# Kernel tuning notes

Hardware: AMD Instinct MI355X
Metric: run time of the kernel (lower is better)

## Reference

```python
import jax, jax.numpy as jnp
import numpy as np

NUM_HEADS = 16
HEAD_DIM = 128  # d_out / num_heads = 2048 / 16
WINDOW = 2048   # sliding_window_size


def setup_inputs() -> dict:
    key = jax.random.key(0)
    kx, kq, kk, kv, ko = jax.random.split(key, 5)
    b, s, d = 2, 2048, 2048
    scale = 0.02
    return {
        "x": jax.random.normal(kx, (b, s, d), dtype=jnp.float32),
        "Wq": jax.random.normal(kq, (d, d), dtype=jnp.float32) * scale,
        "Wk": jax.random.normal(kk, (d, d), dtype=jnp.float32) * scale,
        "Wv": jax.random.normal(kv, (d, d), dtype=jnp.float32) * scale,
        "Wo": jax.random.normal(ko, (d, d), dtype=jnp.float32) * scale,
    }


def reference(x, Wq, Wk, Wv, Wo):
    b, s, _ = x.shape
    H, Dh, W = NUM_HEADS, HEAD_DIM, WINDOW

    # qkv projections (no bias), split into heads: [b, s, H, Dh]
    q = (x @ Wq).reshape(b, s, H, Dh)
    k = (x @ Wk).reshape(b, s, H, Dh)
    v = (x @ Wv).reshape(b, s, H, Dh)

    # attn scores: [b, H, q, k]
    scores = jnp.einsum("bqhd,bkhd->bhqk", q, k)

    # sliding-window mask from absolute positions (fresh cache: q_start=k_start=0)
    pos = jnp.arange(s)
    diff = pos[:, None] - pos[None, :]  # q_pos - k_pos
    mask = (diff < 0) | (diff >= W)
    scores = jnp.where(mask[None, None], -jnp.inf, scores)

    attn = jax.nn.softmax(scores / np.sqrt(Dh).astype(np.float32), axis=-1)

    # context: [b, s, H, Dh] -> [b, s, d_out]
    ctx = jnp.einsum("bhqk,bkhd->bqhd", attn, v).reshape(b, s, H * Dh)
    return ctx @ Wo
```

## Files before the change

kernel.cpp:

```cpp
#include <hip/hip_runtime.h>

typedef __bf16 bf16;
typedef __bf16 bf16x4 __attribute__((ext_vector_type(4)));
typedef __bf16 bf16x8 __attribute__((ext_vector_type(8)));
typedef float f32x4 __attribute__((ext_vector_type(4)));

#define B_ 2
#define S_ 2048
#define D_ 2048
#define H_ 16
#define DH_ 128
#define QKVN 6144

__device__ __forceinline__ void async_load16(const bf16* g, bf16* l) {
    __builtin_amdgcn_global_load_lds((const __attribute__((address_space(1))) void*)g,
                                     (__attribute__((address_space(3))) void*)l, 16, 0, 0);
}

__device__ __forceinline__ unsigned int bf16_bits(float x) {
    bf16 h = (bf16)x;
    return (unsigned int)__builtin_bit_cast(unsigned short, h);
}

__global__ __launch_bounds__(256) void cvt_kernel(const float* __restrict__ src,
                                                  bf16* __restrict__ dst) {
    size_t i = (size_t)blockIdx.x * 256 + threadIdx.x;
    const float4* s = (const float4*)src;
    float4 a = s[2 * i], b = s[2 * i + 1];
    bf16x8 o;
    o[0] = (bf16)a.x; o[1] = (bf16)a.y; o[2] = (bf16)a.z; o[3] = (bf16)a.w;
    o[4] = (bf16)b.x; o[5] = (bf16)b.y; o[6] = (bf16)b.z; o[7] = (bf16)b.w;
    *(bf16x8*)(dst + 8 * i) = o;
}

__global__ __launch_bounds__(256) void wtrans_kernel(const float* __restrict__ Wq,
                                                     const float* __restrict__ Wk,
                                                     const float* __restrict__ Wv,
                                                     const float* __restrict__ Wo,
                                                     bf16* __restrict__ WqkvT,
                                                     bf16* __restrict__ WoT) {
    __shared__ unsigned int tile[64][65];
    int z = blockIdx.z;
    const float* src = (z == 0) ? Wq : (z == 1) ? Wk : (z == 2) ? Wv : Wo;
    bf16* dst = (z < 3) ? (WqkvT + (size_t)z * D_ * D_) : WoT;
    int r0 = blockIdx.y * 64, c0 = blockIdx.x * 64;
    int t = threadIdx.x;
    int tr = t >> 4, tc4 = (t & 15) * 4;
#pragma unroll
    for (int it = 0; it < 4; ++it) {
        int r = it * 16 + tr;
        float4 v = *(const float4*)(src + (size_t)(r0 + r) * D_ + c0 + tc4);
        tile[r][tc4 + 0] = bf16_bits(v.x);
        tile[r][tc4 + 1] = bf16_bits(v.y);
        tile[r][tc4 + 2] = bf16_bits(v.z);
        tile[r][tc4 + 3] = bf16_bits(v.w);
    }
    __syncthreads();
#pragma unroll
    for (int it = 0; it < 4; ++it) {
        int a = it * 16 + tr;
        unsigned u0 = tile[tc4 + 0][a], u1 = tile[tc4 + 1][a];
        unsigned u2 = tile[tc4 + 2][a], u3 = tile[tc4 + 3][a];
        uint2 v;
        v.x = (u0 & 0xffffu) | (u1 << 16);
        v.y = (u2 & 0xffffu) | (u3 << 16);
        *(uint2*)(dst + (size_t)(c0 + a) * D_ + r0 + tc4) = v;
    }
}

__global__ __launch_bounds__(256) void vtrans_kernel(const bf16* __restrict__ qkv,
                                                     bf16* __restrict__ vt) {
    __shared__ unsigned int tile[64][65];
    int bh = blockIdx.z;
    int b = bh >> 4, h = bh & 15;
    int s0 = blockIdx.x * 64, d0 = blockIdx.y * 64;
    int t = threadIdx.x, tr = t >> 4, tc4 = (t & 15) * 4;
#pragma unroll
    for (int it = 0; it < 4; ++it) {
        int r = it * 16 + tr;
        uint2 v = *(const uint2*)(qkv + (size_t)(b * S_ + s0 + r) * QKVN + 2 * D_ + h * DH_ + d0 + tc4);
        tile[r][tc4 + 0] = v.x & 0xffffu;
        tile[r][tc4 + 1] = v.x >> 16;
        tile[r][tc4 + 2] = v.y & 0xffffu;
        tile[r][tc4 + 3] = v.y >> 16;
    }
    __syncthreads();
#pragma unroll
    for (int it = 0; it < 4; ++it) {
        int a = it * 16 + tr;
        unsigned u0 = tile[tc4 + 0][a], u1 = tile[tc4 + 1][a];
        unsigned u2 = tile[tc4 + 2][a], u3 = tile[tc4 + 3][a];
        uint2 v;
        v.x = (u0 & 0xffffu) | (u1 << 16);
        v.y = (u2 & 0xffffu) | (u3 << 16);
        *(uint2*)(vt + (size_t)bh * DH_ * S_ + (size_t)(d0 + a) * S_ + s0 + tc4) = v;
    }
}

template <typename CT>
__global__ __launch_bounds__(256) void gemm_bt(const bf16* __restrict__ A,
                                               const bf16* __restrict__ Bt,
                                               CT* __restrict__ C,
                                               int M, int N, int K) {
    __shared__ __align__(16) bf16 As[128 * 32];
    __shared__ __align__(16) bf16 Bs[128 * 32];
    int t = threadIdx.x;
    int w = t >> 6, l = t & 63;
    int quad = l >> 4, lr = l & 15;
    int wr = w >> 1, wc = w & 1;
    size_t m0 = (size_t)blockIdx.y * 128, n0 = (size_t)blockIdx.x * 128;
    int srow = l >> 2, scol = (l & 3) * 8;

    f32x4 acc[4][4];
#pragma unroll
    for (int i = 0; i < 4; ++i)
#pragma unroll
        for (int j = 0; j < 4; ++j) acc[i][j] = (f32x4){0.f, 0.f, 0.f, 0.f};

    for (int k0 = 0; k0 < K; k0 += 32) {
        __syncthreads();
#pragma unroll
        for (int i = 0; i < 2; ++i) {
            int c = w * 2 + i;
            async_load16(A + (m0 + c * 16 + srow) * (size_t)K + k0 + scol, As + c * 512);
            async_load16(Bt + (n0 + c * 16 + srow) * (size_t)K + k0 + scol, Bs + c * 512);
        }
        asm volatile("s_waitcnt vmcnt(0)" ::: "memory");
        __syncthreads();
        bf16x8 af[4], bfr[4];
#pragma unroll
        for (int i = 0; i < 4; ++i) af[i] = *(const bf16x8*)(As + (wr * 64 + i * 16 + lr) * 32 + quad * 8);
#pragma unroll
        for (int j = 0; j < 4; ++j) bfr[j] = *(const bf16x8*)(Bs + (wc * 64 + j * 16 + lr) * 32 + quad * 8);
#pragma unroll
        for (int i = 0; i < 4; ++i)
#pragma unroll
            for (int j = 0; j < 4; ++j)
                acc[i][j] = __builtin_amdgcn_mfma_f32_16x16x32_bf16(af[i], bfr[j], acc[i][j], 0, 0, 0);
    }

    size_t bm = m0 + wr * 64 + quad * 4;
    size_t bn = n0 + wc * 64 + lr;
#pragma unroll
    for (int i = 0; i < 4; ++i)
#pragma unroll
        for (int j = 0; j < 4; ++j)
#pragma unroll
            for (int r = 0; r < 4; ++r)
                C[(bm + i * 16 + r) * (size_t)N + bn + j * 16] = (CT)acc[i][j][r];
}

#define QK_K 2048
#define QK_N 6144

__device__ __forceinline__ bf16x8 lds_frag(const bf16* tile, int row, int colByte) {
    int off = row * 128 + (colByte ^ ((row & 7) << 4));
    return *(const bf16x8*)((const char*)tile + off);
}

template <int MH, int NH>
__device__ __forceinline__ void mmaq8(f32x4 (&acc)[8][4], const bf16x8 (&afr)[4][2],
                                      const bf16x8 (&bf)[2][2]) {
    __builtin_amdgcn_s_setprio(1);
#pragma unroll
    for (int i = 0; i < 4; ++i)
#pragma unroll
        for (int j = 0; j < 2; ++j)
#pragma unroll
            for (int kk = 0; kk < 2; ++kk)
                acc[MH * 4 + i][NH * 2 + j] = __builtin_amdgcn_mfma_f32_16x16x32_bf16(
                    afr[i][kk], bf[j][kk], acc[MH * 4 + i][NH * 2 + j], 0, 0, 0);
    __builtin_amdgcn_s_setprio(0);
}

__global__ __launch_bounds__(512, 2) void gemm_qkv(const bf16* __restrict__ A,
                                                   const bf16* __restrict__ Bt,
                                                   bf16* __restrict__ C) {
    __shared__ __align__(16) bf16 As[2][256 * 64];
    __shared__ __align__(16) bf16 Bs[2][256 * 64];

    int t = threadIdx.x;
    int wid = t >> 6, lane = t & 63;
    int quad = lane >> 4, lr = lane & 15;
    int wr = wid >> 2, wn = wid & 3;

    int bid = blockIdx.x;
    int swz = (bid & 7) * 48 + (bid >> 3);
    int tn = swz >> 4, tm = swz & 15;
    size_t m0 = (size_t)tm * 256, n0 = (size_t)tn * 256;

    int row_r[2], c8s_r[2];
#pragma unroll
    for (int r = 0; r < 2; ++r) {
        int idx = r * 512 + t;
        row_r[r] = idx >> 3;
        c8s_r[r] = (idx & 7) ^ (row_r[r] & 7);
    }

    auto stA = [&](int kt, int bufi, int h) {
#pragma unroll
        for (int r = 0; r < 2; ++r)
            async_load16(A + (m0 + h * 128 + row_r[r]) * (size_t)QK_K + kt * 64 + c8s_r[r] * 8,
                         &As[bufi][(h * 1024 + r * 512 + wid * 64) * 8]);
    };
    auto stB = [&](int kt, int bufi, int h) {
#pragma unroll
        for (int r = 0; r < 2; ++r)
            async_load16(Bt + (n0 + h * 128 + row_r[r]) * (size_t)QK_K + kt * 64 + c8s_r[r] * 8,
                         &Bs[bufi][(h * 1024 + r * 512 + wid * 64) * 8]);
    };

    f32x4 acc[8][4];
#pragma unroll
    for (int i = 0; i < 8; ++i)
#pragma unroll
        for (int j = 0; j < 4; ++j) acc[i][j] = (f32x4){0.f, 0.f, 0.f, 0.f};

    bf16x8 afr[4][2], bf0[2][2], bf1[2][2];

    auto readA = [&](int bufi, int mh) {
#pragma unroll
        for (int i = 0; i < 4; ++i)
#pragma unroll
            for (int kk = 0; kk < 2; ++kk)
                afr[i][kk] = lds_frag(As[bufi], mh * 128 + wr * 64 + i * 16 + lr, kk * 64 + quad * 16);
    };
    auto readB = [&](int bufi, int nh, bf16x8 (&bf)[2][2]) {
#pragma unroll
        for (int j = 0; j < 2; ++j)
#pragma unroll
            for (int kk = 0; kk < 2; ++kk)
                bf[j][kk] = lds_frag(Bs[bufi], nh * 128 + wn * 32 + j * 16 + lr, kk * 64 + quad * 16);
    };

    stA(0, 0, 0); stB(0, 0, 0); stB(0, 0, 1); stA(0, 0, 1);
    asm volatile("s_waitcnt vmcnt(4)" ::: "memory");
    stA(1, 1, 0); stB(1, 1, 0); stB(1, 1, 1);
    asm volatile("s_waitcnt vmcnt(6)" ::: "memory");
    __builtin_amdgcn_s_barrier();

    for (int it2 = 0; it2 < 15; ++it2) {
        int tt = 2 * it2;
        readA(0, 0);
        readB(0, 0, bf0);
        stA(tt + 1, 1, 1);
        __builtin_amdgcn_s_barrier();
        asm volatile("s_waitcnt lgkmcnt(0)" ::: "memory");
        __builtin_amdgcn_sched_barrier(0);
        mmaq8<0, 0>(acc, afr, bf0);
        __builtin_amdgcn_s_barrier();
        readB(0, 1, bf1);
        stA(tt + 2, 0, 0);
        __builtin_amdgcn_s_barrier();
        asm volatile("s_waitcnt lgkmcnt(0)" ::: "memory");
        __builtin_amdgcn_sched_barrier(0);
        mmaq8<0, 1>(acc, afr, bf1);
        __builtin_amdgcn_s_barrier();
        readA(0, 1);
        stB(tt + 2, 0, 0);
        __builtin_amdgcn_s_barrier();
        asm volatile("s_waitcnt lgkmcnt(0)" ::: "memory");
        __builtin_amdgcn_sched_barrier(0);
        mmaq8<1, 0>(acc, afr, bf0);
        __builtin_amdgcn_s_barrier();
        stB(tt + 2, 0, 1);
        asm volatile("s_waitcnt vmcnt(6)" ::: "memory");
        __builtin_amdgcn_s_barrier();
        mmaq8<1, 1>(acc, afr, bf1);
        __builtin_amdgcn_s_barrier();
        readA(1, 0);
        readB(1, 0, bf0);
        stA(tt + 2, 0, 1);
        __builtin_amdgcn_s_barrier();
        asm volatile("s_waitcnt lgkmcnt(0)" ::: "memory");
        __builtin_amdgcn_sched_barrier(0);
        mmaq8<0, 0>(acc, afr, bf0);
        __builtin_amdgcn_s_barrier();
        readB(1, 1, bf1);
        stA(tt + 3, 1, 0);
        __builtin_amdgcn_s_barrier();
        asm volatile("s_waitcnt lgkmcnt(0)" ::: "memory");
        __builtin_amdgcn_sched_barrier(0);
        mmaq8<0, 1>(acc, afr, bf1);
        __builtin_amdgcn_s_barrier();
        readA(1, 1);
        stB(tt + 3, 1, 0);
        __builtin_amdgcn_s_barrier();
        asm volatile("s_waitcnt lgkmcnt(0)" ::: "memory");
        __builtin_amdgcn_sched_barrier(0);
        mmaq8<1, 0>(acc, afr, bf0);
        __builtin_amdgcn_s_barrier();
        stB(tt + 3, 1, 1);
        asm volatile("s_waitcnt vmcnt(6)" ::: "memory");
        __builtin_amdgcn_s_barrier();
        mmaq8<1, 1>(acc, afr, bf1);
        __builtin_amdgcn_s_barrier();
    }

    {
        readA(0, 0);
        readB(0, 0, bf0);
        stA(31, 1, 1);
        __builtin_amdgcn_s_barrier();
        asm volatile("s_waitcnt lgkmcnt(0)" ::: "memory");
        __builtin_amdgcn_sched_barrier(0);
        mmaq8<0, 0>(acc, afr, bf0);
        __builtin_amdgcn_s_barrier();
        readB(0, 1, bf1);
        __builtin_amdgcn_s_barrier();
        asm volatile("s_waitcnt lgkmcnt(0)" ::: "memory");
        __builtin_amdgcn_sched_barrier(0);
        mmaq8<0, 1>(acc, afr, bf1);
        __builtin_amdgcn_s_barrier();
        readA(0, 1);
        __builtin_amdgcn_s_barrier();
        asm volatile("s_waitcnt lgkmcnt(0)" ::: "memory");
        __builtin_amdgcn_sched_barrier(0);
        mmaq8<1, 0>(acc, afr, bf0);
        __builtin_amdgcn_s_barrier();
        asm volatile("s_waitcnt vmcnt(0)" ::: "memory");
        __builtin_amdgcn_s_barrier();
        mmaq8<1, 1>(acc, afr, bf1);
        __builtin_amdgcn_s_barrier();
        readA(1, 0);
        readB(1, 0, bf0);
        asm volatile("s_waitcnt lgkmcnt(0)" ::: "memory");
        __builtin_amdgcn_sched_barrier(0);
        mmaq8<0, 0>(acc, afr, bf0);
        readB(1, 1, bf1);
        asm volatile("s_waitcnt lgkmcnt(0)" ::: "memory");
        __builtin_amdgcn_sched_barrier(0);
        mmaq8<0, 1>(acc, afr, bf1);
        readA(1, 1);
        asm volatile("s_waitcnt lgkmcnt(0)" ::: "memory");
        __builtin_amdgcn_sched_barrier(0);
        mmaq8<1, 0>(acc, afr, bf0);
        mmaq8<1, 1>(acc, afr, bf1);
    }

#pragma unroll
    for (int mh = 0; mh < 2; ++mh)
#pragma unroll
        for (int i = 0; i < 4; ++i)
#pragma unroll
            for (int nh = 0; nh < 2; ++nh)
#pragma unroll
                for (int j = 0; j < 2; ++j)
#pragma unroll
                    for (int r = 0; r < 4; ++r) {
                        size_t row = m0 + mh * 128 + wr * 64 + i * 16 + quad * 4 + r;
                        size_t col = n0 + nh * 128 + wn * 32 + j * 16 + lr;
                        C[row * QK_N + col] = (bf16)acc[mh * 4 + i][nh * 2 + j][r];
                    }
}

__global__ __launch_bounds__(128) void attn_kernel(const bf16* __restrict__ qkv,
                                                   const bf16* __restrict__ vt,
                                                   bf16* __restrict__ ctx) {
    __shared__ __align__(16) bf16 Ks[2][64 * 128];
    __shared__ __align__(16) bf16 Vts[2][128 * 64];
    __shared__ __align__(16) bf16 Ps[2][32][68];

    int y = blockIdx.y;
    int p = blockIdx.x;
    int b = y >> 4, h = y & 15;
    int t = threadIdx.x, w = t >> 6, l = t & 63;
    int quad = l >> 4, lr = l & 15;

    const bf16* qbase = qkv + (size_t)b * S_ * QKVN + h * DH_;
    const bf16* kbase = qbase + D_;
    const bf16* vbase = vt + (size_t)y * DH_ * S_;

    const int qtA = p, qtB = 31 - p;
    const int nA = p + 1;

    auto stage = [&](int kt, int bi) {
#pragma unroll
        for (int ii = 0; ii < 8; ++ii) {
            int i = 8 * w + ii;
            int row = 4 * i + (l >> 4);
            int cl = (l & 15) ^ (row & 7);
            async_load16(kbase + (size_t)(kt * 64 + row) * QKVN + cl * 8, Ks[bi] + i * 512);
        }
#pragma unroll
        for (int ii = 0; ii < 8; ++ii) {
            int i = 8 * w + ii;
            int dh = 8 * i + (l >> 3);
            int cl = (l & 7) ^ (dh & 7);
            async_load16(vbase + (size_t)dh * S_ + kt * 64 + cl * 8, Vts[bi] + i * 512);
        }
    };

    const float sc2 = 0.12751745f;

    int qt = qtA, q0 = qt * 64;
    bf16x8 qf[2][4];
    auto loadQ = [&]() {
#pragma unroll
        for (int g = 0; g < 2; ++g)
#pragma unroll
            for (int kk = 0; kk < 4; ++kk) {
                bf16x8 raw = *(const bf16x8*)(qbase + (size_t)(q0 + w * 32 + g * 16 + lr) * QKVN + kk * 32 + quad * 8);
#pragma unroll
                for (int e = 0; e < 8; ++e) qf[g][kk][e] = (bf16)((float)raw[e] * sc2);
            }
    };
    loadQ();

    float L_r[2][4];
    f32x4 o[2][8];
#pragma unroll
    for (int g = 0; g < 2; ++g) {
#pragma unroll
        for (int r = 0; r < 4; ++r) L_r[g][r] = 0.f;
#pragma unroll
        for (int nt = 0; nt < 8; ++nt) o[g][nt] = (f32x4){0.f, 0.f, 0.f, 0.f};
    }

    auto epilogue = [&](int q0e) {
#pragma unroll
        for (int g = 0; g < 2; ++g) {
#pragma unroll
            for (int d = 1; d < 16; d <<= 1)
#pragma unroll
                for (int r = 0; r < 4; ++r) L_r[g][r] += __shfl_xor(L_r[g][r], d, 64);
#pragma unroll
            for (int r = 0; r < 4; ++r) {
                float inv = __builtin_amdgcn_rcpf(L_r[g][r]);
                int q = q0e + w * 32 + g * 16 + quad * 4 + r;
#pragma unroll
                for (int nt = 0; nt < 8; ++nt)
                    ctx[(size_t)(b * S_ + q) * D_ + h * DH_ + nt * 16 + lr] = (bf16)(o[g][nt][r] * inv);
            }
        }
    };

    stage(0, 0);

    for (int it = 0; it < 33; ++it) {
        int buf = it & 1;
        asm volatile("s_waitcnt vmcnt(0)" ::: "memory");
        __syncthreads();
        if (it + 1 < 33) {
            int nit = it + 1;
            int nkt = (nit < nA) ? nit : (nit - nA);
            stage(nkt, buf ^ 1);
        }
        int kt = (it < nA) ? it : (it - nA);

        f32x4 s[2][4];
#pragma unroll
        for (int g = 0; g < 2; ++g)
#pragma unroll
            for (int jt = 0; jt < 4; ++jt) s[g][jt] = (f32x4){0.f, 0.f, 0.f, 0.f};
#pragma unroll
        for (int kk = 0; kk < 4; ++kk)
#pragma unroll
            for (int jt = 0; jt < 4; ++jt) {
                bf16x8 kf = *(const bf16x8*)(Ks[buf] + (jt * 16 + lr) * 128 + ((4 * kk + quad) ^ (lr & 7)) * 8);
                s[0][jt] = __builtin_amdgcn_mfma_f32_16x16x32_bf16(qf[0][kk], kf, s[0][jt], 0, 0, 0);
                s[1][jt] = __builtin_amdgcn_mfma_f32_16x16x32_bf16(qf[1][kk], kf, s[1][jt], 0, 0, 0);
            }

        bool diag = (kt == qt);
#pragma unroll
        for (int g = 0; g < 2; ++g) {
#pragma unroll
            for (int jt = 0; jt < 4; ++jt) {
                int keyi = jt * 16 + lr;
#pragma unroll
                for (int r = 0; r < 4; ++r) {
                    float s2 = s[g][jt][r];
                    if (diag && keyi > w * 32 + g * 16 + quad * 4 + r) s2 = -3.0e38f;
                    float pv = __builtin_amdgcn_exp2f(s2);
                    s[g][jt][r] = pv;
                    L_r[g][r] += pv;
                }
            }
#pragma unroll
            for (int jt = 0; jt < 4; ++jt)
#pragma unroll
                for (int r = 0; r < 4; ++r)
                    Ps[w][g * 16 + quad * 4 + r][jt * 16 + lr] = (bf16)s[g][jt][r];
        }
        asm volatile("s_waitcnt lgkmcnt(0)" ::: "memory");

#pragma unroll
        for (int ks = 0; ks < 2; ++ks) {
            bf16x8 pf[2];
#pragma unroll
            for (int g = 0; g < 2; ++g) {
                const bf16* pp = &Ps[w][g * 16 + lr][ks * 32 + quad * 8];
                bf16x4 lo = *(const bf16x4*)pp;
                bf16x4 hi = *(const bf16x4*)(pp + 4);
                pf[g] = __builtin_shufflevector(lo, hi, 0, 1, 2, 3, 4, 5, 6, 7);
            }
#pragma unroll
            for (int nt = 0; nt < 8; ++nt) {
                bf16x8 vf = *(const bf16x8*)(Vts[buf] + (nt * 16 + lr) * 64 + ((4 * ks + quad) ^ (lr & 7)) * 8);
                o[0][nt] = __builtin_amdgcn_mfma_f32_16x16x32_bf16(pf[0], vf, o[0][nt], 0, 0, 0);
                o[1][nt] = __builtin_amdgcn_mfma_f32_16x16x32_bf16(pf[1], vf, o[1][nt], 0, 0, 0);
            }
        }

        if (it == nA - 1) {
            epilogue(q0);
            qt = qtB;
            q0 = qt * 64;
            loadQ();
#pragma unroll
            for (int g = 0; g < 2; ++g) {
#pragma unroll
                for (int r = 0; r < 4; ++r) L_r[g][r] = 0.f;
#pragma unroll
                for (int nt = 0; nt < 8; ++nt) o[g][nt] = (f32x4){0.f, 0.f, 0.f, 0.f};
            }
        }
    }

    epilogue(q0);
}

extern "C" void kernel_launch(void* const* d_in, const int* in_sizes, int n_in,
                              void* d_out, int out_size, void* d_ws, size_t ws_size,
                              hipStream_t stream) {
    const float* x  = (const float*)d_in[0];
    const float* Wq = (const float*)d_in[1];
    const float* Wk = (const float*)d_in[2];
    const float* Wv = (const float*)d_in[3];
    const float* Wo = (const float*)d_in[4];
    float* out = (float*)d_out;

    char* ws = (char*)d_ws;
    bf16* WqkvT = (bf16*)(ws);
    bf16* WoT   = (bf16*)(ws + 25165824);
    bf16* qkv   = (bf16*)(ws + 33554432);
    bf16* vt    = (bf16*)(ws + 83886080);
    bf16* ctx   = (bf16*)(ws + 100663296);
    bf16* xb    = (bf16*)(ws + 117440512);

    cvt_kernel<<<4096, 256, 0, stream>>>(x, xb);
    wtrans_kernel<<<dim3(32, 32, 4), 256, 0, stream>>>(Wq, Wk, Wv, Wo, WqkvT, WoT);
    gemm_qkv<<<dim3(384), 512, 0, stream>>>(xb, WqkvT, qkv);
    vtrans_kernel<<<dim3(32, 2, 32), 256, 0, stream>>>(qkv, vt);
    attn_kernel<<<dim3(16, 32), 128, 0, stream>>>(qkv, vt, ctx);
    gemm_bt<float><<<dim3(16, 32), 256, 0, stream>>>(ctx, WoT, out, B_ * S_, D_, D_);
}
```

Before: 411.8 us.

## Split attention block work across four waves with 16 query rows each

The attention kernel now launches 256 threads (4 waves) per block instead of 128. Each wave handles 16 query rows instead of 32, and the K/V staging loads are spread across twice as many threads. This halves the per-wave register footprint for the O accumulators and scores, which should raise occupancy and latency hiding. In exchange each K/V fragment read from LDS feeds half as many MFMAs, so LDS read traffic per FLOP goes up. An unused NKT constant was also added in the GEMM.

```diff
diff --git a/kernel.cpp b/kernel.cpp
--- a/kernel.cpp
+++ b/kernel.cpp
@@ -239,6 +239,7 @@
     asm volatile("s_waitcnt vmcnt(6)" ::: "memory");
     __builtin_amdgcn_s_barrier();
 
+    const int NKT = QK_K / 64;
     for (int it2 = 0; it2 < 15; ++it2) {
         int tt = 2 * it2;
         readA(0, 0);
@@ -354,12 +355,12 @@
                     }
 }
 
-__global__ __launch_bounds__(128) void attn_kernel(const bf16* __restrict__ qkv,
-                                                   const bf16* __restrict__ vt,
-                                                   bf16* __restrict__ ctx) {
+__global__ __launch_bounds__(256, 2) void attn_kernel(const bf16* __restrict__ qkv,
+                                                      const bf16* __restrict__ vt,
+                                                      bf16* __restrict__ ctx) {
     __shared__ __align__(16) bf16 Ks[2][64 * 128];
     __shared__ __align__(16) bf16 Vts[2][128 * 64];
-    __shared__ __align__(16) bf16 Ps[2][32][68];
+    __shared__ __align__(16) bf16 Ps[4][16][68];
 
     int y = blockIdx.y;
     int p = blockIdx.x;
@@ -376,15 +377,15 @@
 
     auto stage = [&](int kt, int bi) {
 #pragma unroll
-        for (int ii = 0; ii < 8; ++ii) {
-            int i = 8 * w + ii;
+        for (int ii = 0; ii < 4; ++ii) {
+            int i = 4 * w + ii;
             int row = 4 * i + (l >> 4);
             int cl = (l & 15) ^ (row & 7);
             async_load16(kbase + (size_t)(kt * 64 + row) * QKVN + cl * 8, Ks[bi] + i * 512);
         }
 #pragma unroll
-        for (int ii = 0; ii < 8; ++ii) {
-            int i = 8 * w + ii;
+        for (int ii = 0; ii < 4; ++ii) {
+            int i = 4 * w + ii;
             int dh = 8 * i + (l >> 3);
             int cl = (l & 7) ^ (dh & 7);
             async_load16(vbase + (size_t)dh * S_ + kt * 64 + cl * 8, Vts[bi] + i * 512);
@@ -394,44 +395,36 @@
     const float sc2 = 0.12751745f;
 
     int qt = qtA, q0 = qt * 64;
-    bf16x8 qf[2][4];
+    bf16x8 qf[4];
     auto loadQ = [&]() {
 #pragma unroll
-        for (int g = 0; g < 2; ++g)
-#pragma unroll
-            for (int kk = 0; kk < 4; ++kk) {
-                bf16x8 raw = *(const bf16x8*)(qbase + (size_t)(q0 + w * 32 + g * 16 + lr) * QKVN + kk * 32 + quad * 8);
-#pragma unroll
-                for (int e = 0; e < 8; ++e) qf[g][kk][e] = (bf16)((float)raw[e] * sc2);
-            }
+        for (int kk = 0; kk < 4; ++kk) {
+            bf16x8 raw = *(const bf16x8*)(qbase + (size_t)(q0 + w * 16 + lr) * QKVN + kk * 32 + quad * 8);
+#pragma unroll
+            for (int e = 0; e < 8; ++e) qf[kk][e] = (bf16)((float)raw[e] * sc2);
+        }
     };
     loadQ();
 
-    float L_r[2][4];
-    f32x4 o[2][8];
-#pragma unroll
-    for (int g = 0; g < 2; ++g) {
-#pragma unroll
-        for (int r = 0; r < 4; ++r) L_r[g][r] = 0.f;
-#pragma unroll
-        for (int nt = 0; nt < 8; ++nt) o[g][nt] = (f32x4){0.f, 0.f, 0.f, 0.f};
-    }
+    float L_r[4];
+    f32x4 o[8];
+#pragma unroll
+    for (int r = 0; r < 4; ++r) L_r[r] = 0.f;
+#pragma unroll
+    for (int nt = 0; nt < 8; ++nt) o[nt] = (f32x4){0.f, 0.f, 0.f, 0.f};
 
     auto epilogue = [&](int q0e) {
 #pragma unroll
-        for (int g = 0; g < 2; ++g) {
-#pragma unroll
-            for (int d = 1; d < 16; d <<= 1)
-#pragma unroll
-                for (int r = 0; r < 4; ++r) L_r[g][r] += __shfl_xor(L_r[g][r], d, 64);
-#pragma unroll
-            for (int r = 0; r < 4; ++r) {
-                float inv = __builtin_amdgcn_rcpf(L_r[g][r]);
-                int q = q0e + w * 32 + g * 16 + quad * 4 + r;
-#pragma unroll
-                for (int nt = 0; nt < 8; ++nt)
-                    ctx[(size_t)(b * S_ + q) * D_ + h * DH_ + nt * 16 + lr] = (bf16)(o[g][nt][r] * inv);
-            }
+        for (int d = 1; d < 16; d <<= 1)
+#pragma unroll
+            for (int r = 0; r < 4; ++r) L_r[r] += __shfl_xor(L_r[r], d, 64);
+#pragma unroll
+        for (int r = 0; r < 4; ++r) {
+            float inv = __builtin_amdgcn_rcpf(L_r[r]);
+            int q = q0e + w * 16 + quad * 4 + r;
+#pragma unroll
+            for (int nt = 0; nt < 8; ++nt)
+                ctx[(size_t)(b * S_ + q) * D_ + h * DH_ + nt * 16 + lr] = (bf16)(o[nt][r] * inv);
         }
     };
 
@@ -448,58 +441,47 @@
         }
         int kt = (it < nA) ? it : (it - nA);
 
-        f32x4 s[2][4];
-#pragma unroll
-        for (int g = 0; g < 2; ++g)
-#pragma unroll
-            for (int jt = 0; jt < 4; ++jt) s[g][jt] = (f32x4){0.f, 0.f, 0.f, 0.f};
+        f32x4 s[4];
+#pragma unroll
+        for (int jt = 0; jt < 4; ++jt) s[jt] = (f32x4){0.f, 0.f, 0.f, 0.f};
 #pragma unroll
         for (int kk = 0; kk < 4; ++kk)
 #pragma unroll
             for (int jt = 0; jt < 4; ++jt) {
                 bf16x8 kf = *(const bf16x8*)(Ks[buf] + (jt * 16 + lr) * 128 + ((4 * kk + quad) ^ (lr & 7)) * 8);
-                s[0][jt] = __builtin_amdgcn_mfma_f32_16x16x32_bf16(qf[0][kk], kf, s[0][jt], 0, 0, 0);
-                s[1][jt] = __builtin_amdgcn_mfma_f32_16x16x32_bf16(qf[1][kk], kf, s[1][jt], 0, 0, 0);
+                s[jt] = __builtin_amdgcn_mfma_f32_16x16x32_bf16(qf[kk], kf, s[jt], 0, 0, 0);
             }
 
         bool diag = (kt == qt);
 #pragma unroll
-        for (int g = 0; g < 2; ++g) {
-#pragma unroll
-            for (int jt = 0; jt < 4; ++jt) {
-                int keyi = jt * 16 + lr;
-#pragma unroll
-                for (int r = 0; r < 4; ++r) {
-                    float s2 = s[g][jt][r];
-                    if (diag && keyi > w * 32 + g * 16 + quad * 4 + r) s2 = -3.0e38f;
-                    float pv = __builtin_amdgcn_exp2f(s2);
-                    s[g][jt][r] = pv;
-                    L_r[g][r] += pv;
-                }
+        for (int jt = 0; jt < 4; ++jt) {
+            int keyi = jt * 16 + lr;
+#pragma unroll
+            for (int r = 0; r < 4; ++r) {
+                float s2 = s[jt][r];
+                if (diag && keyi > w * 16 + quad * 4 + r) s2 = -3.0e38f;
+                float pv = __builtin_amdgcn_exp2f(s2);
+                s[jt][r] = pv;
+                L_r[r] += pv;
             }
-#pragma unroll
-            for (int jt = 0; jt < 4; ++jt)
-#pragma unroll
-                for (int r = 0; r < 4; ++r)
-                    Ps[w][g * 16 + quad * 4 + r][jt * 16 + lr] = (bf16)s[g][jt][r];
-        }
+        }
+#pragma unroll
+        for (int jt = 0; jt < 4; ++jt)
+#pragma unroll
+            for (int r = 0; r < 4; ++r)
+                Ps[w][quad * 4 + r][jt * 16 + lr] = (bf16)s[jt][r];
         asm volatile("s_waitcnt lgkmcnt(0)" ::: "memory");
 
 #pragma unroll
         for (int ks = 0; ks < 2; ++ks) {
-            bf16x8 pf[2];
-#pragma unroll
-            for (int g = 0; g < 2; ++g) {
-                const bf16* pp = &Ps[w][g * 16 + lr][ks * 32 + quad * 8];
-                bf16x4 lo = *(const bf16x4*)pp;
-                bf16x4 hi = *(const bf16x4*)(pp + 4);
-                pf[g] = __builtin_shufflevector(lo, hi, 0, 1, 2, 3, 4, 5, 6, 7);
-            }
+            const bf16* pp = &Ps[w][lr][ks * 32 + quad * 8];
+            bf16x4 lo = *(const bf16x4*)pp;
+            bf16x4 hi = *(const bf16x4*)(pp + 4);
+            bf16x8 pf = __builtin_shufflevector(lo, hi, 0, 1, 2, 3, 4, 5, 6, 7);
 #pragma unroll
             for (int nt = 0; nt < 8; ++nt) {
                 bf16x8 vf = *(const bf16x8*)(Vts[buf] + (nt * 16 + lr) * 64 + ((4 * ks + quad) ^ (lr & 7)) * 8);
-                o[0][nt] = __builtin_amdgcn_mfma_f32_16x16x32_bf16(pf[0], vf, o[0][nt], 0, 0, 0);
-                o[1][nt] = __builtin_amdgcn_mfma_f32_16x16x32_bf16(pf[1], vf, o[1][nt], 0, 0, 0);
+                o[nt] = __builtin_amdgcn_mfma_f32_16x16x32_bf16(pf, vf, o[nt], 0, 0, 0);
             }
         }
 
@@ -509,12 +491,9 @@
             q0 = qt * 64;
             loadQ();
 #pragma unroll
-            for (int g = 0; g < 2; ++g) {
-#pragma unroll
-                for (int r = 0; r < 4; ++r) L_r[g][r] = 0.f;
-#pragma unroll
-                for (int nt = 0; nt < 8; ++nt) o[g][nt] = (f32x4){0.f, 0.f, 0.f, 0.f};
-            }
+            for (int r = 0; r < 4; ++r) L_r[r] = 0.f;
+#pragma unroll
+            for (int nt = 0; nt < 8; ++nt) o[nt] = (f32x4){0.f, 0.f, 0.f, 0.f};
         }
     }
 
@@ -543,6 +522,6 @@
     wtrans_kernel<<<dim3(32, 32, 4), 256, 0, stream>>>(Wq, Wk, Wv, Wo, WqkvT, WoT);
     gemm_qkv<<<dim3(384), 512, 0, stream>>>(xb, WqkvT, qkv);
     vtrans_kernel<<<dim3(32, 2, 32), 256, 0, stream>>>(qkv, vt);
-    attn_kernel<<<dim3(16, 32), 128, 0, stream>>>(qkv, vt, ctx);
+    attn_kernel<<<dim3(16, 32), 256, 0, stream>>>(qkv, vt, ctx);
     gemm_bt<float><<<dim3(16, 32), 256, 0, stream>>>(ctx, WoT, out, B_ * S_, D_, D_);
 }
```

New measurement: 401.2 us. -2.6%, faster.
